# Kernel tuning notes

Measured on AMD Instinct MI355X. Metric: run time of the kernel, lower is better.

Reference implementation:

```python
import jax, jax.numpy as jnp
import numpy as np

TOP_K = 32
TEMPERATURE = 1.0
PARAM_SCALE = 0.02


def setup_inputs() -> dict:
    key = jax.random.key(0)
    ks = jax.random.split(key, 7)
    B, S, D, F, P, R = 2, 1024, 1024, 4096, 256, 64
    x = jax.random.normal(ks[0], (B, S, D), dtype=jnp.float32)
    fc1_A = jax.random.normal(ks[1], (P, D, R), dtype=jnp.float32) * PARAM_SCALE
    fc1_B = jax.random.normal(ks[2], (P, R, F), dtype=jnp.float32) * PARAM_SCALE
    fc2_A = jax.random.normal(ks[3], (P, F, R), dtype=jnp.float32) * PARAM_SCALE
    fc2_B = jax.random.normal(ks[4], (P, R, D), dtype=jnp.float32) * PARAM_SCALE
    fc1_logits = jax.random.normal(ks[5], (P,), dtype=jnp.float32)
    fc2_logits = jax.random.normal(ks[6], (P,), dtype=jnp.float32)
    return {"x": x, "fc1_A": fc1_A, "fc1_B": fc1_B, "fc2_A": fc2_A,
            "fc2_B": fc2_B, "fc1_logits": fc1_logits, "fc2_logits": fc2_logits}


def _compose_weight(logits, A, B):
    """Top-k select primitives, softmax composition weights, weighted low-rank sum.

    A: (P, d_in, r), B: (P, r, d_out) -> W: (d_in, d_out)
    """
    vals, idx = jax.lax.top_k(logits, TOP_K)          # (K,), (K,)
    w = jax.nn.softmax(vals / TEMPERATURE)            # composition weights over selected
    A_sel = A[idx]                                    # (K, d_in, r) gather
    B_sel = B[idx]                                    # (K, r, d_out) gather
    return jnp.einsum('k,kir,kro->io', w, A_sel, B_sel)


def reference(x, fc1_A, fc1_B, fc2_A, fc2_B, fc1_logits, fc2_logits):
    W1 = _compose_weight(fc1_logits, fc1_A, fc1_B)    # (D, F)
    W2 = _compose_weight(fc2_logits, fc2_A, fc2_B)    # (F, D)
    h = jax.nn.gelu(jnp.einsum('bsd,df->bsf', x, W1))
    return jnp.einsum('bsf,fd->bsd', h, W2)
```

## Files before the change

kernel.cpp:

```cpp
#include <hip/hip_runtime.h>
#include <cstdint>
#include <cstddef>

typedef __attribute__((ext_vector_type(8))) short bhalf8;
typedef __attribute__((ext_vector_type(4))) float f32x4;

__device__ __forceinline__ unsigned short f2bf(float f){
    unsigned int u = __float_as_uint(f);
    u += 0x7fffu + ((u >> 16) & 1u);
    return (unsigned short)(u >> 16);
}

__device__ __forceinline__ float gelu_tanh(float x){
    const float c0 = 0.7978845608028654f;
    float x3 = x * x * x;
    float t = tanhf(c0 * (x + 0.044715f * x3));
    return 0.5f * x * (1.0f + t);
}

__device__ __forceinline__ void async_lds16(const unsigned short* g, unsigned short* l){
    __builtin_amdgcn_global_load_lds(
        (const __attribute__((address_space(1))) void*)g,
        (__attribute__((address_space(3))) void*)l, 16, 0, 0);
}

__global__ void topk_softmax_kernel(const float* __restrict__ lg1,
                                    const float* __restrict__ lg2,
                                    int* __restrict__ idx_out,
                                    float* __restrict__ w_out)
{
    const float* lg = (blockIdx.x == 0) ? lg1 : lg2;
    int*   idxo = idx_out + blockIdx.x * 32;
    float* wo   = w_out   + blockIdx.x * 32;
    const int lane = threadIdx.x;
    float v[4];
    #pragma unroll
    for (int j = 0; j < 4; ++j) v[j] = lg[lane * 4 + j];
    __shared__ float svals[32];
    for (int k = 0; k < 32; ++k){
        float bv = -1e30f; int bi = 0;
        #pragma unroll
        for (int j = 0; j < 4; ++j){
            if (v[j] > bv){ bv = v[j]; bi = lane * 4 + j; }
        }
        for (int off = 32; off > 0; off >>= 1){
            float ov = __shfl_down(bv, off);
            int   oi = __shfl_down(bi, off);
            if (ov > bv){ bv = ov; bi = oi; }
        }
        bv = __shfl(bv, 0);
        bi = __shfl(bi, 0);
        if (lane == 0){ svals[k] = bv; idxo[k] = bi; }
        if ((bi >> 2) == lane) v[bi & 3] = -1e30f;
    }
    if (lane == 0){
        float mx = svals[0];
        float sum = 0.f;
        for (int k = 0; k < 32; ++k){ float e = expf(svals[k] - mx); wo[k] = e; sum += e; }
        float inv = 1.f / sum;
        for (int k = 0; k < 32; ++k) wo[k] *= inv;
    }
}

__global__ void prep_kernel(const float* __restrict__ src,
                            unsigned short* __restrict__ dst,
                            float4* __restrict__ outz)
{
    int b = blockIdx.x;
    if (b < 2048){
        int v = b * 256 + threadIdx.x;
        float4 x = ((const float4*)src)[v];
        ushort4 o; o.x = f2bf(x.x); o.y = f2bf(x.y); o.z = f2bf(x.z); o.w = f2bf(x.w);
        ((ushort4*)dst)[v] = o;
    } else {
        int v = (b - 2048) * 256 + threadIdx.x;
        float4 z = {0.f,0.f,0.f,0.f};
        outz[v] = z;
    }
}

__global__ void gather_nat_kernel(const float* __restrict__ src,
                                  unsigned short* __restrict__ dst,
                                  const int* __restrict__ idx,
                                  const float* __restrict__ w,
                                  int Drows, int use_scale, int n4)
{
    int v = blockIdx.x * 256 + threadIdx.x;
    if (v >= n4) return;
    int c4 = v & 511;
    int d  = v >> 9;
    int k  = c4 >> 4;
    int r4 = c4 & 15;
    int p  = idx[k];
    float sc = use_scale ? w[k] : 1.0f;
    const float4* s = (const float4*)(src + ((size_t)p * Drows + d) * 64) + r4;
    float4 x = *s;
    ushort4 o;
    o.x = f2bf(sc * x.x); o.y = f2bf(sc * x.y);
    o.z = f2bf(sc * x.z); o.w = f2bf(sc * x.w);
    *(ushort4*)(dst + (size_t)d * 2048 + k * 64 + r4 * 4) = o;
}

__global__ void gather_tr_kernel(const float* __restrict__ src,
                                 unsigned short* __restrict__ dst,
                                 const int* __restrict__ idx,
                                 const float* __restrict__ w,
                                 int Fcols, int use_scale)
{
    const int k  = blockIdx.y;
    const int f0 = blockIdx.x * 64;
    const int p  = idx[k];
    const float sc = use_scale ? w[k] : 1.0f;
    __shared__ float tile[64][65];
    const int t  = threadIdx.x;
    const int cf = t & 15;
    const int r0 = t >> 4;
    #pragma unroll
    for (int pass = 0; pass < 4; ++pass){
        int r = r0 + pass * 16;
        float4 x = *((const float4*)(src + ((size_t)p * 64 + r) * Fcols + f0) + cf);
        tile[r][cf * 4 + 0] = x.x; tile[r][cf * 4 + 1] = x.y;
        tile[r][cf * 4 + 2] = x.z; tile[r][cf * 4 + 3] = x.w;
    }
    __syncthreads();
    const int r4  = t & 15;
    const int fl0 = t >> 4;
    #pragma unroll
    for (int pass = 0; pass < 4; ++pass){
        int fl = fl0 + pass * 16;
        ushort4 o;
        o.x = f2bf(sc * tile[r4 * 4 + 0][fl]);
        o.y = f2bf(sc * tile[r4 * 4 + 1][fl]);
        o.z = f2bf(sc * tile[r4 * 4 + 2][fl]);
        o.w = f2bf(sc * tile[r4 * 4 + 3][fl]);
        *(ushort4*)(dst + (size_t)(f0 + fl) * 2048 + k * 64 + r4 * 4) = o;
    }
}

template<int EPI>
__device__ __forceinline__ void gemm_body(unsigned short* smem,
                                          const unsigned short* __restrict__ A,
                                          const unsigned short* __restrict__ Bt,
                                          void* __restrict__ Cout,
                                          int N, int K, int Kslice, int kbeg,
                                          int bm, int bn)
{
    unsigned short* sA0 = smem;
    unsigned short* sA1 = smem + 4096;
    unsigned short* sB0 = smem + 8192;
    unsigned short* sB1 = smem + 12288;
    const int t    = threadIdx.x;
    const int wave = t >> 6;
    const int lane = t & 63;
    const int wr   = (wave >> 1) * 64;
    const int wc   = (wave & 1) * 64;
    const int m16  = lane & 15;
    const int quad = lane >> 4;
    const int srow = t >> 2;
    const int scol = t & 3;

    f32x4 acc[4][4];
    const f32x4 z = {0.f, 0.f, 0.f, 0.f};
    #pragma unroll
    for (int i = 0; i < 4; ++i)
        #pragma unroll
        for (int j = 0; j < 4; ++j) acc[i][j] = z;

    const unsigned short* Arow = A  + (size_t)(bm + srow) * K + scol * 8 + kbeg;
    const unsigned short* Brow = Bt + (size_t)(bn + srow) * K + scol * 8 + kbeg;
    const size_t rstep = (size_t)64 * K;
    unsigned short* lA0 = sA0 + t * 8;
    unsigned short* lA1 = sA1 + t * 8;
    unsigned short* lB0 = sB0 + t * 8;
    unsigned short* lB1 = sB1 + t * 8;

    for (int k0 = 0; k0 < Kslice; k0 += 64){
        async_lds16(Arow + k0,              lA0);
        async_lds16(Arow + rstep + k0,      lA0 + 64 * 32);
        async_lds16(Arow + k0 + 32,         lA1);
        async_lds16(Arow + rstep + k0 + 32, lA1 + 64 * 32);
        async_lds16(Brow + k0,              lB0);
        async_lds16(Brow + rstep + k0,      lB0 + 64 * 32);
        async_lds16(Brow + k0 + 32,         lB1);
        async_lds16(Brow + rstep + k0 + 32, lB1 + 64 * 32);
        __syncthreads();

        bhalf8 af0[4], bf0[4], af1[4], bf1[4];
        #pragma unroll
        for (int i = 0; i < 4; ++i){
            af0[i] = *(const bhalf8*)(sA0 + (wr + i * 16 + m16) * 32 + quad * 8);
            af1[i] = *(const bhalf8*)(sA1 + (wr + i * 16 + m16) * 32 + quad * 8);
        }
        #pragma unroll
        for (int j = 0; j < 4; ++j){
            bf0[j] = *(const bhalf8*)(sB0 + (wc + j * 16 + m16) * 32 + quad * 8);
            bf1[j] = *(const bhalf8*)(sB1 + (wc + j * 16 + m16) * 32 + quad * 8);
        }

        #pragma unroll
        for (int i = 0; i < 4; ++i)
            #pragma unroll
            for (int j = 0; j < 4; ++j)
                acc[i][j] = __builtin_amdgcn_mfma_f32_16x16x32_bf16(af0[i], bf0[j], acc[i][j], 0, 0, 0);
        #pragma unroll
        for (int i = 0; i < 4; ++i)
            #pragma unroll
            for (int j = 0; j < 4; ++j)
                acc[i][j] = __builtin_amdgcn_mfma_f32_16x16x32_bf16(af1[i], bf1[j], acc[i][j], 0, 0, 0);
        __syncthreads();
    }

    #pragma unroll
    for (int i = 0; i < 4; ++i){
        #pragma unroll
        for (int j = 0; j < 4; ++j){
            #pragma unroll
            for (int r = 0; r < 4; ++r){
                int row = bm + wr + i * 16 + quad * 4 + r;
                int col = bn + wc + j * 16 + m16;
                float vv = acc[i][j][r];
                if (EPI == 1) vv = gelu_tanh(vv);
                if (EPI == 3) atomicAdd(&((float*)Cout)[(size_t)row * N + col], vv);
                else ((unsigned short*)Cout)[(size_t)row * N + col] = f2bf(vv);
            }
        }
    }
}

__launch_bounds__(256, 2)
__global__ void gemm13_kernel(const unsigned short* __restrict__ A1,
                              const unsigned short* __restrict__ B1,
                              unsigned short* __restrict__ C1,
                              const unsigned short* __restrict__ A2,
                              const unsigned short* __restrict__ B2,
                              unsigned short* __restrict__ C2)
{
    __shared__ unsigned short smem[4 * 128 * 32];
    int id = blockIdx.x;
    if (id < 256){
        gemm_body<0>(smem, A1, B1, C1, 1024, 2048, 2048, 0,
                     (id >> 3) * 128, (id & 7) * 128);
    } else {
        id -= 256;
        gemm_body<0>(smem, A2, B2, C2, 4096, 2048, 2048, 0,
                     (id >> 5) * 128, (id & 31) * 128);
    }
}

template<int EPI>
__launch_bounds__(256, 2)
__global__ void gemm_nt_kernel(const unsigned short* __restrict__ A,
                               const unsigned short* __restrict__ Bt,
                               void* __restrict__ Cout,
                               int N, int K, int Kslice)
{
    __shared__ unsigned short smem[4 * 128 * 32];
    gemm_body<EPI>(smem, A, Bt, Cout, N, K, Kslice, blockIdx.z * Kslice,
                   blockIdx.y * 128, blockIdx.x * 128);
}

extern "C" void kernel_launch(void* const* d_in, const int* in_sizes, int n_in,
                              void* d_out, int out_size, void* d_ws, size_t ws_size,
                              hipStream_t stream)
{
    const float* x    = (const float*)d_in[0];
    const float* fc1A = (const float*)d_in[1];
    const float* fc1B = (const float*)d_in[2];
    const float* fc2A = (const float*)d_in[3];
    const float* fc2B = (const float*)d_in[4];
    const float* lg1  = (const float*)d_in[5];
    const float* lg2  = (const float*)d_in[6];
    float* out = (float*)d_out;

    char* ws = (char*)d_ws;
    int*            idxb = (int*)(ws + 0);
    float*          wb   = (float*)(ws + 256);
    char* base = ws + 4096;
    unsigned short* x16  = (unsigned short*)(base);
    unsigned short* Ag1  = (unsigned short*)(base + (4ull  << 20));
    unsigned short* Bt1  = (unsigned short*)(base + (8ull  << 20));
    unsigned short* Ag2  = (unsigned short*)(base + (24ull << 20));
    unsigned short* Bg2t = (unsigned short*)(base + (40ull << 20));
    unsigned short* W1t  = (unsigned short*)(base + (44ull << 20));
    unsigned short* W2t  = (unsigned short*)(base + (52ull << 20));
    unsigned short* hbuf = (unsigned short*)(base + (60ull << 20));

    topk_softmax_kernel<<<dim3(2), dim3(64), 0, stream>>>(lg1, lg2, idxb, wb);

    prep_kernel<<<dim3(4096), dim3(256), 0, stream>>>(x, x16, (float4*)out);

    gather_nat_kernel<<<dim3(2048), dim3(256), 0, stream>>>(fc1A, Ag1, idxb, wb, 1024, 1, 524288);
    gather_tr_kernel<<<dim3(64, 32), dim3(256), 0, stream>>>(fc1B, Bt1, idxb, wb, 4096, 0);
    gather_nat_kernel<<<dim3(8192), dim3(256), 0, stream>>>(fc2A, Ag2, idxb + 32, wb + 32, 4096, 0, 2097152);
    gather_tr_kernel<<<dim3(16, 32), dim3(256), 0, stream>>>(fc2B, Bg2t, idxb + 32, wb + 32, 1024, 1);

    gemm13_kernel<<<dim3(512), dim3(256), 0, stream>>>(Bt1, Ag1, W1t, Bg2t, Ag2, W2t);

    gemm_nt_kernel<1><<<dim3(32, 16), dim3(256), 0, stream>>>(x16, W1t, hbuf, 4096, 1024, 1024);

    gemm_nt_kernel<3><<<dim3(8, 16, 4), dim3(256), 0, stream>>>(hbuf, W2t, out, 1024, 4096, 1024);
}
```

Before: 611.1 us.

## Fuse prep/gather kernels, swizzle blocks across XCDs, replace atomic split-K with reduction

Merges x conversion and the four weight gather kernels into one launch, and drops the zeroing of the output. Adds an XCD-aware block-index swizzle to the GEMM kernels. Replaces atomicAdd split-K in the final GEMM with per-slice partial buffers plus a separate reduce kernel. Top-k softmax normalization is now parallelized across lanes. This trades 32 MB of extra partial-buffer traffic against the atomics and the launch overhead.

Measured after the change: 589.5 us. 3.5% less time.

```diff
diff --git a/kernel.cpp b/kernel.cpp
--- a/kernel.cpp
+++ b/kernel.cpp
@@ -48,79 +48,72 @@
             int   oi = __shfl_down(bi, off);
             if (ov > bv){ bv = ov; bi = oi; }
         }
-        bv = __shfl(bv, 0);
         bi = __shfl(bi, 0);
         if (lane == 0){ svals[k] = bv; idxo[k] = bi; }
         if ((bi >> 2) == lane) v[bi & 3] = -1e30f;
     }
-    if (lane == 0){
-        float mx = svals[0];
-        float sum = 0.f;
-        for (int k = 0; k < 32; ++k){ float e = expf(svals[k] - mx); wo[k] = e; sum += e; }
-        float inv = 1.f / sum;
-        for (int k = 0; k < 32; ++k) wo[k] *= inv;
-    }
-}
-
-__global__ void prep_kernel(const float* __restrict__ src,
-                            unsigned short* __restrict__ dst,
-                            float4* __restrict__ outz)
-{
+    float sv = svals[lane & 31];
+    float e  = expf(sv - svals[0]);
+    float s  = e;
+    #pragma unroll
+    for (int off = 16; off > 0; off >>= 1) s += __shfl_xor(s, off);
+    if (lane < 32) wo[lane] = e / s;
+}
+
+__global__ void prep_gather_kernel(const float* __restrict__ x,  unsigned short* __restrict__ x16,
+                                   const float* __restrict__ fc1A, unsigned short* __restrict__ Ag1,
+                                   const float* __restrict__ fc1B, unsigned short* __restrict__ Bt1,
+                                   const float* __restrict__ fc2A, unsigned short* __restrict__ Ag2,
+                                   const float* __restrict__ fc2B, unsigned short* __restrict__ Bg2t,
+                                   const int* __restrict__ idxb, const float* __restrict__ wb)
+{
+    __shared__ float tile[64][65];
+    const int t = threadIdx.x;
     int b = blockIdx.x;
+
     if (b < 2048){
-        int v = b * 256 + threadIdx.x;
-        float4 x = ((const float4*)src)[v];
-        ushort4 o; o.x = f2bf(x.x); o.y = f2bf(x.y); o.z = f2bf(x.z); o.w = f2bf(x.w);
-        ((ushort4*)dst)[v] = o;
-    } else {
-        int v = (b - 2048) * 256 + threadIdx.x;
-        float4 z = {0.f,0.f,0.f,0.f};
-        outz[v] = z;
-    }
-}
-
-__global__ void gather_nat_kernel(const float* __restrict__ src,
-                                  unsigned short* __restrict__ dst,
-                                  const int* __restrict__ idx,
-                                  const float* __restrict__ w,
-                                  int Drows, int use_scale, int n4)
-{
-    int v = blockIdx.x * 256 + threadIdx.x;
-    if (v >= n4) return;
-    int c4 = v & 511;
-    int d  = v >> 9;
-    int k  = c4 >> 4;
-    int r4 = c4 & 15;
-    int p  = idx[k];
-    float sc = use_scale ? w[k] : 1.0f;
-    const float4* s = (const float4*)(src + ((size_t)p * Drows + d) * 64) + r4;
-    float4 x = *s;
-    ushort4 o;
-    o.x = f2bf(sc * x.x); o.y = f2bf(sc * x.y);
-    o.z = f2bf(sc * x.z); o.w = f2bf(sc * x.w);
-    *(ushort4*)(dst + (size_t)d * 2048 + k * 64 + r4 * 4) = o;
-}
-
-__global__ void gather_tr_kernel(const float* __restrict__ src,
-                                 unsigned short* __restrict__ dst,
-                                 const int* __restrict__ idx,
-                                 const float* __restrict__ w,
-                                 int Fcols, int use_scale)
-{
-    const int k  = blockIdx.y;
-    const int f0 = blockIdx.x * 64;
+        int v = b * 256 + t;
+        float4 xx = ((const float4*)x)[v];
+        ushort4 o; o.x=f2bf(xx.x); o.y=f2bf(xx.y); o.z=f2bf(xx.z); o.w=f2bf(xx.w);
+        ((ushort4*)x16)[v] = o;
+        return;
+    }
+    b -= 2048;
+    if (b < 10240){
+        const float* src; unsigned short* dst; const int* idx; const float* w;
+        int Drows, use_scale, v;
+        if (b < 2048){ src=fc1A; dst=Ag1; idx=idxb;    w=wb;    Drows=1024; use_scale=1; v=b*256+t; }
+        else         { src=fc2A; dst=Ag2; idx=idxb+32; w=wb+32; Drows=4096; use_scale=0; v=(b-2048)*256+t; }
+        int c4 = v & 511;
+        int d  = v >> 9;
+        int k  = c4 >> 4;
+        int r4 = c4 & 15;
+        int p  = idx[k];
+        float sc = use_scale ? w[k] : 1.0f;
+        float4 xx = *((const float4*)(src + ((size_t)p * Drows + d) * 64) + r4);
+        ushort4 o;
+        o.x = f2bf(sc * xx.x); o.y = f2bf(sc * xx.y);
+        o.z = f2bf(sc * xx.z); o.w = f2bf(sc * xx.w);
+        *(ushort4*)(dst + (size_t)d * 2048 + k * 64 + r4 * 4) = o;
+        return;
+    }
+    b -= 10240;
+    const float* src; unsigned short* dst; const int* idx; const float* w;
+    int Fcols, use_scale;
+    if (b < 2048){ src=fc1B; dst=Bt1;  idx=idxb;    w=wb;    Fcols=4096; use_scale=0; }
+    else         { src=fc2B; dst=Bg2t; idx=idxb+32; w=wb+32; Fcols=1024; use_scale=1; b -= 2048; }
+    const int k  = b & 31;
+    const int f0 = (b >> 5) * 64;
     const int p  = idx[k];
     const float sc = use_scale ? w[k] : 1.0f;
-    __shared__ float tile[64][65];
-    const int t  = threadIdx.x;
     const int cf = t & 15;
     const int r0 = t >> 4;
     #pragma unroll
     for (int pass = 0; pass < 4; ++pass){
         int r = r0 + pass * 16;
-        float4 x = *((const float4*)(src + ((size_t)p * 64 + r) * Fcols + f0) + cf);
-        tile[r][cf * 4 + 0] = x.x; tile[r][cf * 4 + 1] = x.y;
-        tile[r][cf * 4 + 2] = x.z; tile[r][cf * 4 + 3] = x.w;
+        float4 xx = *((const float4*)(src + ((size_t)p * 64 + r) * Fcols + f0) + cf);
+        tile[r][cf * 4 + 0] = xx.x; tile[r][cf * 4 + 1] = xx.y;
+        tile[r][cf * 4 + 2] = xx.z; tile[r][cf * 4 + 3] = xx.w;
     }
     __syncthreads();
     const int r4  = t & 15;
@@ -220,12 +213,14 @@
                 int col = bn + wc + j * 16 + m16;
                 float vv = acc[i][j][r];
                 if (EPI == 1) vv = gelu_tanh(vv);
-                if (EPI == 3) atomicAdd(&((float*)Cout)[(size_t)row * N + col], vv);
+                if (EPI == 2) ((float*)Cout)[(size_t)row * N + col] = vv;
                 else ((unsigned short*)Cout)[(size_t)row * N + col] = f2bf(vv);
             }
         }
     }
 }
+
+__device__ __forceinline__ int xcd_swz512(int id){ return (id & 7) * 64 + (id >> 3); }
 
 __launch_bounds__(256, 2)
 __global__ void gemm13_kernel(const unsigned short* __restrict__ A1,
@@ -236,7 +231,7 @@
                               unsigned short* __restrict__ C2)
 {
     __shared__ unsigned short smem[4 * 128 * 32];
-    int id = blockIdx.x;
+    int id = xcd_swz512(blockIdx.x);
     if (id < 256){
         gemm_body<0>(smem, A1, B1, C1, 1024, 2048, 2048, 0,
                      (id >> 3) * 128, (id & 7) * 128);
@@ -247,16 +242,42 @@
     }
 }
 
-template<int EPI>
 __launch_bounds__(256, 2)
-__global__ void gemm_nt_kernel(const unsigned short* __restrict__ A,
-                               const unsigned short* __restrict__ Bt,
-                               void* __restrict__ Cout,
-                               int N, int K, int Kslice)
+__global__ void gemm2_kernel(const unsigned short* __restrict__ A,
+                             const unsigned short* __restrict__ Bt,
+                             unsigned short* __restrict__ C)
 {
     __shared__ unsigned short smem[4 * 128 * 32];
-    gemm_body<EPI>(smem, A, Bt, Cout, N, K, Kslice, blockIdx.z * Kslice,
-                   blockIdx.y * 128, blockIdx.x * 128);
+    int id = xcd_swz512(blockIdx.x);
+    gemm_body<1>(smem, A, Bt, C, 4096, 1024, 1024, 0,
+                 (id >> 5) * 128, (id & 31) * 128);
+}
+
+__launch_bounds__(256, 2)
+__global__ void gemm4_kernel(const unsigned short* __restrict__ A,
+                             const unsigned short* __restrict__ Bt,
+                             float* __restrict__ part)
+{
+    __shared__ unsigned short smem[4 * 128 * 32];
+    int id = xcd_swz512(blockIdx.x);
+    int bz = id >> 7;
+    int r  = id & 127;
+    float* Cs = part + (size_t)bz * (2048 * 1024);
+    gemm_body<2>(smem, A, Bt, Cs, 1024, 4096, 1024, bz * 1024,
+                 (r >> 3) * 128, (r & 7) * 128);
+}
+
+__global__ void reduce4_kernel(const float4* __restrict__ p, float4* __restrict__ out)
+{
+    const int S = 524288;
+    int v = blockIdx.x * 256 + threadIdx.x;
+    float4 a = p[v], b = p[v + S], c = p[v + 2 * S], d = p[v + 3 * S];
+    float4 r;
+    r.x = (a.x + b.x) + (c.x + d.x);
+    r.y = (a.y + b.y) + (c.y + d.y);
+    r.z = (a.z + b.z) + (c.z + d.z);
+    r.w = (a.w + b.w) + (c.w + d.w);
+    out[v] = r;
 }
 
 extern "C" void kernel_launch(void* const* d_in, const int* in_sizes, int n_in,
@@ -284,19 +305,18 @@
     unsigned short* W1t  = (unsigned short*)(base + (44ull << 20));
     unsigned short* W2t  = (unsigned short*)(base + (52ull << 20));
     unsigned short* hbuf = (unsigned short*)(base + (60ull << 20));
+    float*          part = (float*)(base + (76ull << 20));
 
     topk_softmax_kernel<<<dim3(2), dim3(64), 0, stream>>>(lg1, lg2, idxb, wb);
 
-    prep_kernel<<<dim3(4096), dim3(256), 0, stream>>>(x, x16, (float4*)out);
-
-    gather_nat_kernel<<<dim3(2048), dim3(256), 0, stream>>>(fc1A, Ag1, idxb, wb, 1024, 1, 524288);
-    gather_tr_kernel<<<dim3(64, 32), dim3(256), 0, stream>>>(fc1B, Bt1, idxb, wb, 4096, 0);
-    gather_nat_kernel<<<dim3(8192), dim3(256), 0, stream>>>(fc2A, Ag2, idxb + 32, wb + 32, 4096, 0, 2097152);
-    gather_tr_kernel<<<dim3(16, 32), dim3(256), 0, stream>>>(fc2B, Bg2t, idxb + 32, wb + 32, 1024, 1);
+    prep_gather_kernel<<<dim3(14848), dim3(256), 0, stream>>>(
+        x, x16, fc1A, Ag1, fc1B, Bt1, fc2A, Ag2, fc2B, Bg2t, idxb, wb);
 
     gemm13_kernel<<<dim3(512), dim3(256), 0, stream>>>(Bt1, Ag1, W1t, Bg2t, Ag2, W2t);
 
-    gemm_nt_kernel<1><<<dim3(32, 16), dim3(256), 0, stream>>>(x16, W1t, hbuf, 4096, 1024, 1024);
-
-    gemm_nt_kernel<3><<<dim3(8, 16, 4), dim3(256), 0, stream>>>(hbuf, W2t, out, 1024, 4096, 1024);
-}
+    gemm2_kernel<<<dim3(512), dim3(256), 0, stream>>>(x16, W1t, hbuf);
+
+    gemm4_kernel<<<dim3(512), dim3(256), 0, stream>>>(hbuf, W2t, part);
+
+    reduce4_kernel<<<dim3(2048), dim3(256), 0, stream>>>((const float4*)part, (float4*)out);
+}
```
